# Kernel optimization log

Measured on AMD Instinct MI355X. Metric: run time of the kernel, lower is better.

## Reference

```python
import jax, jax.numpy as jnp
import numpy as np

B, N, F_IN, H, MH, STEPS = 8192, 9, 15, 128, 256, 4
E_PER = 16
MASK_IDX = jnp.arange(8)  # mask = [True]*8 + [False]


def setup_inputs() -> dict:
    key = jax.random.key(0)
    ks = jax.random.split(key, 24)
    s = 0.05
    inp = {
        "obs": jax.random.normal(ks[0], (B, 135), jnp.float32),
        "edges": jax.random.randint(ks[1], (B, 2, E_PER), 0, N, jnp.int32),
        "enc_W": jax.random.normal(ks[2], (F_IN, H), jnp.float32) * s,
        "enc_b": jax.random.normal(ks[3], (H,), jnp.float32) * s,
        "msg_W1": jax.random.normal(ks[4], (STEPS, 2 * H, MH), jnp.float32) * s,
        "msg_b1": jax.random.normal(ks[5], (STEPS, MH), jnp.float32) * s,
        "msg_W2": jax.random.normal(ks[6], (STEPS, MH, MH), jnp.float32) * s,
        "msg_b2": jax.random.normal(ks[7], (STEPS, MH), jnp.float32) * s,
        "msg_W3": jax.random.normal(ks[8], (STEPS, MH, H), jnp.float32) * s,
        "msg_b3": jax.random.normal(ks[9], (STEPS, H), jnp.float32) * s,
        "gru_Wi": jax.random.normal(ks[10], (STEPS, H, 3 * H), jnp.float32) * s,
        "gru_Wh": jax.random.normal(ks[11], (STEPS, H, 3 * H), jnp.float32) * s,
        "gru_bi": jax.random.normal(ks[12], (STEPS, 3 * H), jnp.float32) * s,
        "gru_bh": jax.random.normal(ks[13], (STEPS, 3 * H), jnp.float32) * s,
        "dec_W1": jax.random.normal(ks[14], (H, MH), jnp.float32) * s,
        "dec_b1": jax.random.normal(ks[15], (MH,), jnp.float32) * s,
        "dec_W2": jax.random.normal(ks[16], (MH, MH), jnp.float32) * s,
        "dec_b2": jax.random.normal(ks[17], (MH,), jnp.float32) * s,
        "dec_W3": jax.random.normal(ks[18], (MH, 1), jnp.float32) * s,
        "dec_b3": jax.random.normal(ks[19], (1,), jnp.float32) * s,
    }
    return inp


def reference(obs, edges, enc_W, enc_b, msg_W1, msg_b1, msg_W2, msg_b2,
              msg_W3, msg_b3, gru_Wi, gru_Wh, gru_bi, gru_bh,
              dec_W1, dec_b1, dec_W2, dec_b2, dec_W3, dec_b3):
    BN = B * N
    x = obs.reshape(BN, F_IN)                       # [B*N, 15]
    x = jnp.tanh(x @ enc_W + enc_b)                 # encoder -> [B*N, H]

    # flatten per-graph edges into a global edge list, then add self-loops
    offsets = (jnp.arange(B, dtype=jnp.int32) * N)[:, None, None]
    eg = edges + offsets                            # [B, 2, 16]
    loops = jnp.arange(BN, dtype=jnp.int32)
    src = jnp.concatenate([eg[:, 0, :].reshape(-1), loops])  # x_j (source)
    dst = jnp.concatenate([eg[:, 1, :].reshape(-1), loops])  # x_i (target)
    deg = jax.ops.segment_sum(jnp.ones_like(dst, dtype=x.dtype), dst,
                              num_segments=BN)      # >=1 due to self-loops

    for s in range(STEPS):
        m = jnp.concatenate([x[dst], x[src]], axis=-1)       # [E, 2H]
        m = jnp.tanh(m @ msg_W1[s] + msg_b1[s])
        m = jnp.tanh(m @ msg_W2[s] + msg_b2[s])
        m = m @ msg_W3[s] + msg_b3[s]                        # [E, H]
        aggr = jax.ops.segment_sum(m, dst, num_segments=BN) / deg[:, None]
        # GRUCell(input=aggr, hidden=x), PyTorch gate order (r, z, n)
        gi = aggr @ gru_Wi[s] + gru_bi[s]
        gh = x @ gru_Wh[s] + gru_bh[s]
        ir, iz, inn = jnp.split(gi, 3, axis=-1)
        hr, hz, hn = jnp.split(gh, 3, axis=-1)
        r = jax.nn.sigmoid(ir + hr)
        z = jax.nn.sigmoid(iz + hz)
        n = jnp.tanh(inn + r * hn)
        x = (1.0 - z) * n + z * x

    d = jnp.tanh(x @ dec_W1 + dec_b1)
    d = jnp.tanh(d @ dec_W2 + dec_b2)
    d = d @ dec_W3 + dec_b3                                  # [B*N, 1]
    out = d.reshape(B, N)
    return out[:, MASK_IDX]                                  # [B, 8]
```

## Files before the change

### kernel.cpp

```cpp
#include <hip/hip_runtime.h>
#include <hip/hip_bf16.h>
#include <math.h>

#define BGR   8192
#define NND   9
#define BN    73728
#define NE    131072
#define ETOT  204800
#define H     128
#define MH    256
#define FIN   15

typedef __bf16 bf16_t;
typedef bf16_t bf16x8 __attribute__((ext_vector_type(8)));
typedef float  f32x4  __attribute__((ext_vector_type(4)));

__device__ __forceinline__ unsigned short f2bf(float f) {
    unsigned int u = __float_as_uint(f);
    u += 0x7fff + ((u >> 16) & 1);
    return (unsigned short)(u >> 16);
}
__device__ __forceinline__ bf16x8 as_frag(int4 v) {
    union { int4 i; bf16x8 f; } u; u.i = v; return u.f;
}
__device__ __forceinline__ float fast_tanh(float v) {
    float e = __expf(2.0f * v);
    return 1.0f - __fdividef(2.0f, e + 1.0f);
}
__device__ __forceinline__ int sw_off(int m, int k) {
    return m * 256 + ((((k >> 3) ^ (m & 7)) << 3) | (k & 7));
}

__global__ void deg_kernel(const int* __restrict__ edges, float* __restrict__ inv_deg) {
    int g = blockIdx.x * 256 + threadIdx.x;
    if (g >= BGR) return;
    int cnt[NND];
#pragma unroll
    for (int n = 0; n < NND; ++n) cnt[n] = 1;
    for (int j = 0; j < 16; ++j) {
        int d = edges[g * 32 + 16 + j];
#pragma unroll
        for (int n = 0; n < NND; ++n) cnt[n] += (d == n) ? 1 : 0;
    }
#pragma unroll
    for (int n = 0; n < NND; ++n) inv_deg[g * NND + n] = 1.0f / (float)cnt[n];
}

__global__ void enc_kernel(const float* __restrict__ obs, const float* __restrict__ W,
                           const float* __restrict__ b, float* __restrict__ x) {
    int tid = blockIdx.x * 256 + threadIdx.x;
    int i = tid >> 7, h = tid & 127;
    float acc = b[h];
#pragma unroll
    for (int k = 0; k < FIN; ++k) acc += obs[i * FIN + k] * W[k * H + h];
    x[i * H + h] = tanhf(acc);
}

__global__ void wt_kernel(const float* __restrict__ W1, const float* __restrict__ W2,
                          const float* __restrict__ W3, const float* __restrict__ Wi,
                          const float* __restrict__ Wh, unsigned short* __restrict__ out) {
    int idx = blockIdx.x * 256 + threadIdx.x;
    float v;
    if (idx < 262144) {
        int s = idx >> 16, r = idx & 65535, n = r >> 8, k = r & 255;
        v = W1[(s << 16) + (k << 8) + n];
    } else if (idx < 524288) {
        int i2 = idx - 262144;
        int s = i2 >> 16, r = i2 & 65535, n = r >> 8, k = r & 255;
        v = W2[(s << 16) + (k << 8) + n];
    } else if (idx < 655360) {
        int i3 = idx - 524288;
        int s = i3 >> 15, r = i3 & 32767, n = r >> 8, k = r & 255;
        v = W3[(s << 15) + (k << 7) + n];
    } else {
        int i4 = idx - 655360;
        int s = i4 >> 17, rr = i4 & 131071;
        int p = rr >> 8, k = rr & 255;
        int w = p >> 7, rem = p & 127;
        int gate = rem >> 5, hh = (rem >> 4) & 1, c = rem & 15;
        int h = w * 32 + hh * 16 + c;
        const int sb = s * 49152;
        if (gate == 0)      v = (k < 128) ? Wi[sb + k * 384 + h]       : Wh[sb + (k - 128) * 384 + h];
        else if (gate == 1) v = (k < 128) ? Wi[sb + k * 384 + 128 + h] : Wh[sb + (k - 128) * 384 + 128 + h];
        else if (gate == 2) v = (k < 128) ? Wi[sb + k * 384 + 256 + h] : 0.f;
        else                v = (k < 128) ? 0.f                        : Wh[sb + (k - 128) * 384 + 256 + h];
    }
    out[idx] = f2bf(v);
}

__global__ __launch_bounds__(256, 2) void msg_mfma(
        const float* __restrict__ x, const int* __restrict__ edges,
        const unsigned short* __restrict__ W1T, const float* __restrict__ b1,
        const unsigned short* __restrict__ W2T, const float* __restrict__ b2,
        const unsigned short* __restrict__ W3T, const float* __restrict__ b3,
        float* __restrict__ aggr) {
    __shared__ unsigned short bufA[64 * 256];
    __shared__ unsigned short bufB[64 * 256];
    const int t  = threadIdx.x;
    const int e0 = blockIdx.x * 64;
    const int wv = t >> 6;
    const int ln = t & 63;
    const int lrow = ln & 15;
    const int lq   = ln >> 4;

    {
        const int row  = t >> 1;
        const int e    = row & 63;
        const int side = row >> 6;
        const int eg   = e0 + e;
        int node;
        if (eg < NE) {
            int g = eg >> 4, j = eg & 15;
            node = g * NND + (side ? edges[g * 32 + j] : edges[g * 32 + 16 + j]);
        } else {
            node = eg - NE;
        }
        const int kpart = (t & 1) * 64;
        const float* xs = x + (size_t)node * H + kpart;
        const int kbase = side * 128 + kpart;
#pragma unroll
        for (int i = 0; i < 16; ++i) {
            float4 v = *(const float4*)(xs + i * 4);
            int k0 = kbase + i * 4;
            ushort4 o;
            o.x = f2bf(v.x); o.y = f2bf(v.y); o.z = f2bf(v.z); o.w = f2bf(v.w);
            *(ushort4*)(bufA + sw_off(e, k0)) = o;
        }
    }
    __syncthreads();

    const f32x4 zero = {0.f, 0.f, 0.f, 0.f};
    const int nbase = wv * 64;

    {
        f32x4 acc[4][4];
#pragma unroll
        for (int i = 0; i < 4; ++i)
#pragma unroll
            for (int j = 0; j < 4; ++j) acc[i][j] = zero;
        for (int kq = 0; kq < 8; ++kq) {
            const int ko = kq * 32 + lq * 8;
            bf16x8 af[4], bfr[4];
#pragma unroll
            for (int tm = 0; tm < 4; ++tm)
                af[tm] = as_frag(*(const int4*)(bufA + sw_off(tm * 16 + lrow, ko)));
#pragma unroll
            for (int tn = 0; tn < 4; ++tn)
                bfr[tn] = as_frag(*(const int4*)(W1T + (size_t)(nbase + tn * 16 + lrow) * 256 + ko));
#pragma unroll
            for (int tm = 0; tm < 4; ++tm)
#pragma unroll
                for (int tn = 0; tn < 4; ++tn)
                    acc[tm][tn] = __builtin_amdgcn_mfma_f32_16x16x32_bf16(af[tm], bfr[tn], acc[tm][tn], 0, 0, 0);
        }
#pragma unroll
        for (int tn = 0; tn < 4; ++tn) {
            const int n = nbase + tn * 16 + lrow;
            const float bias = b1[n];
#pragma unroll
            for (int tm = 0; tm < 4; ++tm)
#pragma unroll
                for (int r = 0; r < 4; ++r) {
                    const int m = tm * 16 + lq * 4 + r;
                    bufB[sw_off(m, n)] = f2bf(fast_tanh(acc[tm][tn][r] + bias));
                }
        }
    }
    __syncthreads();

    {
        f32x4 acc[4][4];
#pragma unroll
        for (int i = 0; i < 4; ++i)
#pragma unroll
            for (int j = 0; j < 4; ++j) acc[i][j] = zero;
        for (int kq = 0; kq < 8; ++kq) {
            const int ko = kq * 32 + lq * 8;
            bf16x8 af[4], bfr[4];
#pragma unroll
            for (int tm = 0; tm < 4; ++tm)
                af[tm] = as_frag(*(const int4*)(bufB + sw_off(tm * 16 + lrow, ko)));
#pragma unroll
            for (int tn = 0; tn < 4; ++tn)
                bfr[tn] = as_frag(*(const int4*)(W2T + (size_t)(nbase + tn * 16 + lrow) * 256 + ko));
#pragma unroll
            for (int tm = 0; tm < 4; ++tm)
#pragma unroll
                for (int tn = 0; tn < 4; ++tn)
                    acc[tm][tn] = __builtin_amdgcn_mfma_f32_16x16x32_bf16(af[tm], bfr[tn], acc[tm][tn], 0, 0, 0);
        }
#pragma unroll
        for (int tn = 0; tn < 4; ++tn) {
            const int n = nbase + tn * 16 + lrow;
            const float bias = b2[n];
#pragma unroll
            for (int tm = 0; tm < 4; ++tm)
#pragma unroll
                for (int r = 0; r < 4; ++r) {
                    const int m = tm * 16 + lq * 4 + r;
                    bufA[sw_off(m, n)] = f2bf(fast_tanh(acc[tm][tn][r] + bias));
                }
        }
    }
    __syncthreads();

    {
        const int mh = wv >> 1;
        const int nh = wv & 1;
        f32x4 acc[2][4];
#pragma unroll
        for (int i = 0; i < 2; ++i)
#pragma unroll
            for (int j = 0; j < 4; ++j) acc[i][j] = zero;
        for (int kq = 0; kq < 8; ++kq) {
            const int ko = kq * 32 + lq * 8;
            bf16x8 af[2], bfr[4];
#pragma unroll
            for (int tm = 0; tm < 2; ++tm)
                af[tm] = as_frag(*(const int4*)(bufA + sw_off(mh * 32 + tm * 16 + lrow, ko)));
#pragma unroll
            for (int tn = 0; tn < 4; ++tn)
                bfr[tn] = as_frag(*(const int4*)(W3T + (size_t)(nh * 64 + tn * 16 + lrow) * 256 + ko));
#pragma unroll
            for (int tm = 0; tm < 2; ++tm)
#pragma unroll
                for (int tn = 0; tn < 4; ++tn)
                    acc[tm][tn] = __builtin_amdgcn_mfma_f32_16x16x32_bf16(af[tm], bfr[tn], acc[tm][tn], 0, 0, 0);
        }
#pragma unroll
        for (int tm = 0; tm < 2; ++tm)
#pragma unroll
            for (int r = 0; r < 4; ++r) {
                const int m = mh * 32 + tm * 16 + lq * 4 + r;
                const int eg = e0 + m;
                int d;
                if (eg < NE) {
                    int g = eg >> 4;
                    d = g * NND + edges[g * 32 + 16 + (eg & 15)];
                } else {
                    d = eg - NE;
                }
                float* ap = aggr + (size_t)d * H;
#pragma unroll
                for (int tn = 0; tn < 4; ++tn) {
                    const int n = nh * 64 + tn * 16 + lrow;
                    atomicAdd(ap + n, acc[tm][tn][r] + b3[n]);
                }
            }
    }
}

__global__ __launch_bounds__(256, 2) void gru_mfma(
        float* __restrict__ x, float* __restrict__ aggr, const float* __restrict__ inv_deg,
        const unsigned short* __restrict__ WG,
        const float* __restrict__ bi, const float* __restrict__ bh) {
    __shared__ unsigned short bufA[64 * 256];
    const int t = threadIdx.x;
    const int n0 = blockIdx.x * 64;
    const int wv = t >> 6, ln = t & 63, lrow = ln & 15, lq = ln >> 4;

    {
        const int m = t >> 2;
        const int q = t & 3;
        const int node = n0 + m;
        const int k0 = q * 64;
        const float scale = (q < 2) ? inv_deg[node] : 1.f;
        const float* src = (q < 2) ? (aggr + (size_t)node * H + k0)
                                   : (x    + (size_t)node * H + (k0 - 128));
#pragma unroll
        for (int i = 0; i < 16; ++i) {
            float4 v = *(const float4*)(src + i * 4);
            ushort4 o;
            o.x = f2bf(v.x * scale); o.y = f2bf(v.y * scale);
            o.z = f2bf(v.z * scale); o.w = f2bf(v.w * scale);
            *(ushort4*)(bufA + sw_off(m, k0 + i * 4)) = o;
        }
    }
    __syncthreads();

    const f32x4 zero = {0.f, 0.f, 0.f, 0.f};
    f32x4 acc[4][8];
#pragma unroll
    for (int i = 0; i < 4; ++i)
#pragma unroll
        for (int j = 0; j < 8; ++j) acc[i][j] = zero;

    for (int kq = 0; kq < 8; ++kq) {
        const int ko = kq * 32 + lq * 8;
        bf16x8 af[4], bfr[8];
#pragma unroll
        for (int tm = 0; tm < 4; ++tm)
            af[tm] = as_frag(*(const int4*)(bufA + sw_off(tm * 16 + lrow, ko)));
#pragma unroll
        for (int jt = 0; jt < 8; ++jt)
            bfr[jt] = as_frag(*(const int4*)(WG + (size_t)(wv * 128 + jt * 16 + lrow) * 256 + ko));
#pragma unroll
        for (int tm = 0; tm < 4; ++tm)
#pragma unroll
            for (int jt = 0; jt < 8; ++jt)
                acc[tm][jt] = __builtin_amdgcn_mfma_f32_16x16x32_bf16(af[tm], bfr[jt], acc[tm][jt], 0, 0, 0);
    }

#pragma unroll
    for (int hh = 0; hh < 2; ++hh) {
        const int h = wv * 32 + hh * 16 + lrow;
        const float b_r = bi[h] + bh[h];
        const float b_z = bi[128 + h] + bh[128 + h];
        const float b_n = bi[256 + h];
        const float b_h = bh[256 + h];
#pragma unroll
        for (int tm = 0; tm < 4; ++tm) {
#pragma unroll
            for (int r = 0; r < 4; ++r) {
                const int node = n0 + tm * 16 + lq * 4 + r;
                const float irhr = acc[tm][0 + hh][r] + b_r;
                const float izhz = acc[tm][2 + hh][r] + b_z;
                const float inn  = acc[tm][4 + hh][r] + b_n;
                const float hn   = acc[tm][6 + hh][r] + b_h;
                const float rg = 1.f / (1.f + expf(-irhr));
                const float zg = 1.f / (1.f + expf(-izhz));
                const float ng = tanhf(inn + rg * hn);
                const float xo = x[(size_t)node * H + h];
                x[(size_t)node * H + h] = (1.f - zg) * ng + zg * xo;
                aggr[(size_t)node * H + h] = 0.f;
            }
        }
    }
}

__global__ __launch_bounds__(256, 2) void dec_kernel(
        const float* __restrict__ x,
        const float* __restrict__ W1, const float* __restrict__ b1,
        const float* __restrict__ W2, const float* __restrict__ b2,
        const float* __restrict__ W3, const float* __restrict__ b3,
        float* __restrict__ out) {
    __shared__ float bufA[256 * 36];
    __shared__ float d1[256 * 36];
    const int t = threadIdx.x;
    const int id0 = blockIdx.x * 32;

    {
        const int n = t & 31;
        const int k0 = (t >> 5) * 16;
        const int id = id0 + n;
        const int node = (id >> 3) * NND + (id & 7);
#pragma unroll
        for (int i = 0; i < 16; ++i)
            bufA[(k0 + i) * 36 + n] = x[node * H + k0 + i];
    }
    __syncthreads();

    const int cg = t & 63, ng = t >> 6;
    const int c0 = cg * 4, nb = ng * 8;
    float acc[32];

#pragma unroll
    for (int i = 0; i < 32; ++i) acc[i] = 0.f;
    for (int k = 0; k < 128; ++k) {
        const float4 w  = *(const float4*)(W1 + k * 256 + c0);
        const float4 a0 = *(const float4*)(bufA + k * 36 + nb);
        const float4 a1 = *(const float4*)(bufA + k * 36 + nb + 4);
        const float wv[4] = {w.x, w.y, w.z, w.w};
        const float av[8] = {a0.x, a0.y, a0.z, a0.w, a1.x, a1.y, a1.z, a1.w};
#pragma unroll
        for (int cc = 0; cc < 4; ++cc)
#pragma unroll
            for (int j = 0; j < 8; ++j) acc[cc * 8 + j] += wv[cc] * av[j];
    }
    __syncthreads();
#pragma unroll
    for (int cc = 0; cc < 4; ++cc) {
        float bv = b1[c0 + cc];
#pragma unroll
        for (int j = 0; j < 8; ++j)
            d1[(c0 + cc) * 36 + nb + j] = tanhf(acc[cc * 8 + j] + bv);
    }
    __syncthreads();

#pragma unroll
    for (int i = 0; i < 32; ++i) acc[i] = 0.f;
    for (int k = 0; k < 256; ++k) {
        const float4 w  = *(const float4*)(W2 + k * 256 + c0);
        const float4 a0 = *(const float4*)(d1 + k * 36 + nb);
        const float4 a1 = *(const float4*)(d1 + k * 36 + nb + 4);
        const float wv[4] = {w.x, w.y, w.z, w.w};
        const float av[8] = {a0.x, a0.y, a0.z, a0.w, a1.x, a1.y, a1.z, a1.w};
#pragma unroll
        for (int cc = 0; cc < 4; ++cc)
#pragma unroll
            for (int j = 0; j < 8; ++j) acc[cc * 8 + j] += wv[cc] * av[j];
    }
#pragma unroll
    for (int cc = 0; cc < 4; ++cc) {
        float bv = b2[c0 + cc];
#pragma unroll
        for (int j = 0; j < 8; ++j)
            bufA[(c0 + cc) * 36 + nb + j] = tanhf(acc[cc * 8 + j] + bv);
    }
    __syncthreads();

    {
        const int n3 = t >> 3, p = t & 7;
        float s = 0.f;
#pragma unroll
        for (int i = 0; i < 32; ++i) {
            int k = p * 32 + i;
            s += bufA[k * 36 + n3] * W3[k];
        }
        s += __shfl_down(s, 4, 8);
        s += __shfl_down(s, 2, 8);
        s += __shfl_down(s, 1, 8);
        if (p == 0) out[id0 + n3] = s + b3[0];
    }
}

extern "C" void kernel_launch(void* const* d_in, const int* in_sizes, int n_in,
                              void* d_out, int out_size, void* d_ws, size_t ws_size,
                              hipStream_t stream) {
    const float* obs    = (const float*)d_in[0];
    const int*   edges  = (const int*)  d_in[1];
    const float* enc_W  = (const float*)d_in[2];
    const float* enc_b  = (const float*)d_in[3];
    const float* msg_W1 = (const float*)d_in[4];
    const float* msg_b1 = (const float*)d_in[5];
    const float* msg_W2 = (const float*)d_in[6];
    const float* msg_b2 = (const float*)d_in[7];
    const float* msg_W3 = (const float*)d_in[8];
    const float* msg_b3 = (const float*)d_in[9];
    const float* gru_Wi = (const float*)d_in[10];
    const float* gru_Wh = (const float*)d_in[11];
    const float* gru_bi = (const float*)d_in[12];
    const float* gru_bh = (const float*)d_in[13];
    const float* dec_W1 = (const float*)d_in[14];
    const float* dec_b1 = (const float*)d_in[15];
    const float* dec_W2 = (const float*)d_in[16];
    const float* dec_b2 = (const float*)d_in[17];
    const float* dec_W3 = (const float*)d_in[18];
    const float* dec_b3 = (const float*)d_in[19];

    float* x       = (float*)d_ws;
    float* aggr    = x + (size_t)BN * H;
    float* inv_deg = aggr + (size_t)BN * H;
    unsigned short* wbf = (unsigned short*)(inv_deg + BN);

    hipMemsetAsync(aggr, 0, (size_t)BN * H * sizeof(float), stream);
    deg_kernel<<<(BGR + 255) / 256, 256, 0, stream>>>(edges, inv_deg);
    wt_kernel<<<1179648 / 256, 256, 0, stream>>>(msg_W1, msg_W2, msg_W3, gru_Wi, gru_Wh, wbf);
    enc_kernel<<<BN * H / 256, 256, 0, stream>>>(obs, enc_W, enc_b, x);

    for (int s = 0; s < 4; ++s) {
        const unsigned short* W1T = wbf + (size_t)s * 65536;
        const unsigned short* W2T = wbf + 262144 + (size_t)s * 65536;
        const unsigned short* W3T = wbf + 524288 + (size_t)s * 32768;
        const unsigned short* WGs = wbf + 655360 + (size_t)s * 131072;
        msg_mfma<<<ETOT / 64, 256, 0, stream>>>(
            x, edges,
            W1T, msg_b1 + (size_t)s * 256,
            W2T, msg_b2 + (size_t)s * 256,
            W3T, msg_b3 + (size_t)s * 128,
            aggr);
        gru_mfma<<<BN / 64, 256, 0, stream>>>(
            x, aggr, inv_deg, WGs,
            gru_bi + (size_t)s * 384, gru_bh + (size_t)s * 384);
    }

    dec_kernel<<<BGR * 8 / 32, 256, 0, stream>>>(
        x, dec_W1, dec_b1, dec_W2, dec_b2, dec_W3, dec_b3, (float*)d_out);
}
```

Before: 1.646 ms.

## Port decoder to bf16 MFMA, halve msg LDS, move bias b3 into GRU

The fp32 scalar decoder becomes a bf16 MFMA kernel, with its weights pre-transposed to bf16 in wt_kernel. msg_mfma drops from two LDS buffers to one, using extra barriers so it can run 4 blocks per CU instead of 2. The msg_b3 bias is no longer added inside every per-edge atomicAdd; it is applied once per node in gru_mfma's load phase as aggr*inv_deg + b3, which is algebraically equivalent because the average over degree includes the bias once. Packed bf16 conversion intrinsics replace the per-element rounding, and the decoder now runs at bf16 precision, which adds numerical error.

```diff
diff --git a/kernel.cpp b/kernel.cpp
--- a/kernel.cpp
+++ b/kernel.cpp
@@ -20,6 +20,11 @@
     u += 0x7fff + ((u >> 16) & 1);
     return (unsigned short)(u >> 16);
 }
+__device__ __forceinline__ unsigned int pkbf(float a, float b) {
+    union { __hip_bfloat162 h; unsigned int u; } un;
+    un.h = __float22bfloat162_rn(make_float2(a, b));
+    return un.u;
+}
 __device__ __forceinline__ bf16x8 as_frag(int4 v) {
     union { int4 i; bf16x8 f; } u; u.i = v; return u.f;
 }
@@ -58,7 +63,8 @@
 
 __global__ void wt_kernel(const float* __restrict__ W1, const float* __restrict__ W2,
                           const float* __restrict__ W3, const float* __restrict__ Wi,
-                          const float* __restrict__ Wh, unsigned short* __restrict__ out) {
+                          const float* __restrict__ Wh, const float* __restrict__ dW1,
+                          const float* __restrict__ dW2, unsigned short* __restrict__ out) {
     int idx = blockIdx.x * 256 + threadIdx.x;
     float v;
     if (idx < 262144) {
@@ -72,7 +78,7 @@
         int i3 = idx - 524288;
         int s = i3 >> 15, r = i3 & 32767, n = r >> 8, k = r & 255;
         v = W3[(s << 15) + (k << 7) + n];
-    } else {
+    } else if (idx < 1179648) {
         int i4 = idx - 655360;
         int s = i4 >> 17, rr = i4 & 131071;
         int p = rr >> 8, k = rr & 255;
@@ -84,18 +90,25 @@
         else if (gate == 1) v = (k < 128) ? Wi[sb + k * 384 + 128 + h] : Wh[sb + (k - 128) * 384 + 128 + h];
         else if (gate == 2) v = (k < 128) ? Wi[sb + k * 384 + 256 + h] : 0.f;
         else                v = (k < 128) ? 0.f                        : Wh[sb + (k - 128) * 384 + 256 + h];
+    } else if (idx < 1212416) {
+        int i5 = idx - 1179648;
+        int n = i5 >> 7, k = i5 & 127;
+        v = dW1[k * 256 + n];
+    } else {
+        int i6 = idx - 1212416;
+        int n = i6 >> 8, k = i6 & 255;
+        v = dW2[k * 256 + n];
     }
     out[idx] = f2bf(v);
 }
 
-__global__ __launch_bounds__(256, 2) void msg_mfma(
+__global__ __launch_bounds__(256, 4) void msg_mfma(
         const float* __restrict__ x, const int* __restrict__ edges,
         const unsigned short* __restrict__ W1T, const float* __restrict__ b1,
         const unsigned short* __restrict__ W2T, const float* __restrict__ b2,
-        const unsigned short* __restrict__ W3T, const float* __restrict__ b3,
+        const unsigned short* __restrict__ W3T,
         float* __restrict__ aggr) {
-    __shared__ unsigned short bufA[64 * 256];
-    __shared__ unsigned short bufB[64 * 256];
+    __shared__ unsigned short buf[64 * 256];
     const int t  = threadIdx.x;
     const int e0 = blockIdx.x * 64;
     const int wv = t >> 6;
@@ -121,10 +134,9 @@
 #pragma unroll
         for (int i = 0; i < 16; ++i) {
             float4 v = *(const float4*)(xs + i * 4);
-            int k0 = kbase + i * 4;
-            ushort4 o;
-            o.x = f2bf(v.x); o.y = f2bf(v.y); o.z = f2bf(v.z); o.w = f2bf(v.w);
-            *(ushort4*)(bufA + sw_off(e, k0)) = o;
+            uint2 o;
+            o.x = pkbf(v.x, v.y); o.y = pkbf(v.z, v.w);
+            *(uint2*)(buf + sw_off(e, kbase + i * 4)) = o;
         }
     }
     __syncthreads();
@@ -143,7 +155,7 @@
             bf16x8 af[4], bfr[4];
 #pragma unroll
             for (int tm = 0; tm < 4; ++tm)
-                af[tm] = as_frag(*(const int4*)(bufA + sw_off(tm * 16 + lrow, ko)));
+                af[tm] = as_frag(*(const int4*)(buf + sw_off(tm * 16 + lrow, ko)));
 #pragma unroll
             for (int tn = 0; tn < 4; ++tn)
                 bfr[tn] = as_frag(*(const int4*)(W1T + (size_t)(nbase + tn * 16 + lrow) * 256 + ko));
@@ -153,6 +165,7 @@
                 for (int tn = 0; tn < 4; ++tn)
                     acc[tm][tn] = __builtin_amdgcn_mfma_f32_16x16x32_bf16(af[tm], bfr[tn], acc[tm][tn], 0, 0, 0);
         }
+        __syncthreads();
 #pragma unroll
         for (int tn = 0; tn < 4; ++tn) {
             const int n = nbase + tn * 16 + lrow;
@@ -162,7 +175,7 @@
 #pragma unroll
                 for (int r = 0; r < 4; ++r) {
                     const int m = tm * 16 + lq * 4 + r;
-                    bufB[sw_off(m, n)] = f2bf(fast_tanh(acc[tm][tn][r] + bias));
+                    buf[sw_off(m, n)] = f2bf(fast_tanh(acc[tm][tn][r] + bias));
                 }
         }
     }
@@ -179,7 +192,7 @@
             bf16x8 af[4], bfr[4];
 #pragma unroll
             for (int tm = 0; tm < 4; ++tm)
-                af[tm] = as_frag(*(const int4*)(bufB + sw_off(tm * 16 + lrow, ko)));
+                af[tm] = as_frag(*(const int4*)(buf + sw_off(tm * 16 + lrow, ko)));
 #pragma unroll
             for (int tn = 0; tn < 4; ++tn)
                 bfr[tn] = as_frag(*(const int4*)(W2T + (size_t)(nbase + tn * 16 + lrow) * 256 + ko));
@@ -189,6 +202,7 @@
                 for (int tn = 0; tn < 4; ++tn)
                     acc[tm][tn] = __builtin_amdgcn_mfma_f32_16x16x32_bf16(af[tm], bfr[tn], acc[tm][tn], 0, 0, 0);
         }
+        __syncthreads();
 #pragma unroll
         for (int tn = 0; tn < 4; ++tn) {
             const int n = nbase + tn * 16 + lrow;
@@ -198,7 +212,7 @@
 #pragma unroll
                 for (int r = 0; r < 4; ++r) {
                     const int m = tm * 16 + lq * 4 + r;
-                    bufA[sw_off(m, n)] = f2bf(fast_tanh(acc[tm][tn][r] + bias));
+                    buf[sw_off(m, n)] = f2bf(fast_tanh(acc[tm][tn][r] + bias));
                 }
         }
     }
@@ -217,7 +231,7 @@
             bf16x8 af[2], bfr[4];
 #pragma unroll
             for (int tm = 0; tm < 2; ++tm)
-                af[tm] = as_frag(*(const int4*)(bufA + sw_off(mh * 32 + tm * 16 + lrow, ko)));
+                af[tm] = as_frag(*(const int4*)(buf + sw_off(mh * 32 + tm * 16 + lrow, ko)));
 #pragma unroll
             for (int tn = 0; tn < 4; ++tn)
                 bfr[tn] = as_frag(*(const int4*)(W3T + (size_t)(nh * 64 + tn * 16 + lrow) * 256 + ko));
@@ -244,7 +258,7 @@
 #pragma unroll
                 for (int tn = 0; tn < 4; ++tn) {
                     const int n = nh * 64 + tn * 16 + lrow;
-                    atomicAdd(ap + n, acc[tm][tn][r] + b3[n]);
+                    atomicAdd(ap + n, acc[tm][tn][r]);
                 }
             }
     }
@@ -252,7 +266,7 @@
 
 __global__ __launch_bounds__(256, 2) void gru_mfma(
         float* __restrict__ x, float* __restrict__ aggr, const float* __restrict__ inv_deg,
-        const unsigned short* __restrict__ WG,
+        const unsigned short* __restrict__ WG, const float* __restrict__ b3m,
         const float* __restrict__ bi, const float* __restrict__ bh) {
     __shared__ unsigned short bufA[64 * 256];
     const int t = threadIdx.x;
@@ -264,16 +278,26 @@
         const int q = t & 3;
         const int node = n0 + m;
         const int k0 = q * 64;
-        const float scale = (q < 2) ? inv_deg[node] : 1.f;
-        const float* src = (q < 2) ? (aggr + (size_t)node * H + k0)
-                                   : (x    + (size_t)node * H + (k0 - 128));
-#pragma unroll
-        for (int i = 0; i < 16; ++i) {
-            float4 v = *(const float4*)(src + i * 4);
-            ushort4 o;
-            o.x = f2bf(v.x * scale); o.y = f2bf(v.y * scale);
-            o.z = f2bf(v.z * scale); o.w = f2bf(v.w * scale);
-            *(ushort4*)(bufA + sw_off(m, k0 + i * 4)) = o;
+        if (q < 2) {
+            const float scale = inv_deg[node];
+            const float* src = aggr + (size_t)node * H + k0;
+#pragma unroll
+            for (int i = 0; i < 16; ++i) {
+                float4 v = *(const float4*)(src + i * 4);
+                const float4 bb = *(const float4*)(b3m + k0 + i * 4);
+                v.x = v.x * scale + bb.x; v.y = v.y * scale + bb.y;
+                v.z = v.z * scale + bb.z; v.w = v.w * scale + bb.w;
+                uint2 o; o.x = pkbf(v.x, v.y); o.y = pkbf(v.z, v.w);
+                *(uint2*)(bufA + sw_off(m, k0 + i * 4)) = o;
+            }
+        } else {
+            const float* src = x + (size_t)node * H + (k0 - 128);
+#pragma unroll
+            for (int i = 0; i < 16; ++i) {
+                float4 v = *(const float4*)(src + i * 4);
+                uint2 o; o.x = pkbf(v.x, v.y); o.y = pkbf(v.z, v.w);
+                *(uint2*)(bufA + sw_off(m, k0 + i * 4)) = o;
+            }
         }
     }
     __syncthreads();
@@ -328,89 +352,120 @@
     }
 }
 
-__global__ __launch_bounds__(256, 2) void dec_kernel(
+__global__ __launch_bounds__(256, 4) void dec_mfma(
         const float* __restrict__ x,
-        const float* __restrict__ W1, const float* __restrict__ b1,
-        const float* __restrict__ W2, const float* __restrict__ b2,
+        const unsigned short* __restrict__ W1T, const float* __restrict__ b1,
+        const unsigned short* __restrict__ W2T, const float* __restrict__ b2,
         const float* __restrict__ W3, const float* __restrict__ b3,
         float* __restrict__ out) {
-    __shared__ float bufA[256 * 36];
-    __shared__ float d1[256 * 36];
+    __shared__ unsigned short buf[64 * 256];
     const int t = threadIdx.x;
-    const int id0 = blockIdx.x * 32;
-
-    {
-        const int n = t & 31;
-        const int k0 = (t >> 5) * 16;
-        const int id = id0 + n;
+    const int id0 = blockIdx.x * 64;
+    const int wv = t >> 6, ln = t & 63, lrow = ln & 15, lq = ln >> 4;
+    const int nbase = wv * 64;
+
+    {
+        const int m = t >> 2, q = t & 3;
+        const int id = id0 + m;
         const int node = (id >> 3) * NND + (id & 7);
-#pragma unroll
-        for (int i = 0; i < 16; ++i)
-            bufA[(k0 + i) * 36 + n] = x[node * H + k0 + i];
-    }
-    __syncthreads();
-
-    const int cg = t & 63, ng = t >> 6;
-    const int c0 = cg * 4, nb = ng * 8;
-    float acc[32];
-
-#pragma unroll
-    for (int i = 0; i < 32; ++i) acc[i] = 0.f;
-    for (int k = 0; k < 128; ++k) {
-        const float4 w  = *(const float4*)(W1 + k * 256 + c0);
-        const float4 a0 = *(const float4*)(bufA + k * 36 + nb);
-        const float4 a1 = *(const float4*)(bufA + k * 36 + nb + 4);
-        const float wv[4] = {w.x, w.y, w.z, w.w};
-        const float av[8] = {a0.x, a0.y, a0.z, a0.w, a1.x, a1.y, a1.z, a1.w};
-#pragma unroll
-        for (int cc = 0; cc < 4; ++cc)
-#pragma unroll
-            for (int j = 0; j < 8; ++j) acc[cc * 8 + j] += wv[cc] * av[j];
-    }
-    __syncthreads();
-#pragma unroll
-    for (int cc = 0; cc < 4; ++cc) {
-        float bv = b1[c0 + cc];
-#pragma unroll
-        for (int j = 0; j < 8; ++j)
-            d1[(c0 + cc) * 36 + nb + j] = tanhf(acc[cc * 8 + j] + bv);
-    }
-    __syncthreads();
-
-#pragma unroll
-    for (int i = 0; i < 32; ++i) acc[i] = 0.f;
-    for (int k = 0; k < 256; ++k) {
-        const float4 w  = *(const float4*)(W2 + k * 256 + c0);
-        const float4 a0 = *(const float4*)(d1 + k * 36 + nb);
-        const float4 a1 = *(const float4*)(d1 + k * 36 + nb + 4);
-        const float wv[4] = {w.x, w.y, w.z, w.w};
-        const float av[8] = {a0.x, a0.y, a0.z, a0.w, a1.x, a1.y, a1.z, a1.w};
-#pragma unroll
-        for (int cc = 0; cc < 4; ++cc)
-#pragma unroll
-            for (int j = 0; j < 8; ++j) acc[cc * 8 + j] += wv[cc] * av[j];
-    }
-#pragma unroll
-    for (int cc = 0; cc < 4; ++cc) {
-        float bv = b2[c0 + cc];
-#pragma unroll
-        for (int j = 0; j < 8; ++j)
-            bufA[(c0 + cc) * 36 + nb + j] = tanhf(acc[cc * 8 + j] + bv);
-    }
-    __syncthreads();
-
-    {
-        const int n3 = t >> 3, p = t & 7;
+        const float* src = x + (size_t)node * H + q * 32;
+#pragma unroll
+        for (int i = 0; i < 8; ++i) {
+            float4 v = *(const float4*)(src + i * 4);
+            uint2 o; o.x = pkbf(v.x, v.y); o.y = pkbf(v.z, v.w);
+            *(uint2*)(buf + sw_off(m, q * 32 + i * 4)) = o;
+        }
+    }
+    __syncthreads();
+
+    const f32x4 zero = {0.f, 0.f, 0.f, 0.f};
+
+    {
+        f32x4 acc[4][4];
+#pragma unroll
+        for (int i = 0; i < 4; ++i)
+#pragma unroll
+            for (int j = 0; j < 4; ++j) acc[i][j] = zero;
+        for (int kq = 0; kq < 4; ++kq) {
+            const int ko = kq * 32 + lq * 8;
+            bf16x8 af[4], bfr[4];
+#pragma unroll
+            for (int tm = 0; tm < 4; ++tm)
+                af[tm] = as_frag(*(const int4*)(buf + sw_off(tm * 16 + lrow, ko)));
+#pragma unroll
+            for (int tn = 0; tn < 4; ++tn)
+                bfr[tn] = as_frag(*(const int4*)(W1T + (size_t)(nbase + tn * 16 + lrow) * 128 + ko));
+#pragma unroll
+            for (int tm = 0; tm < 4; ++tm)
+#pragma unroll
+                for (int tn = 0; tn < 4; ++tn)
+                    acc[tm][tn] = __builtin_amdgcn_mfma_f32_16x16x32_bf16(af[tm], bfr[tn], acc[tm][tn], 0, 0, 0);
+        }
+        __syncthreads();
+#pragma unroll
+        for (int tn = 0; tn < 4; ++tn) {
+            const int n = nbase + tn * 16 + lrow;
+            const float bias = b1[n];
+#pragma unroll
+            for (int tm = 0; tm < 4; ++tm)
+#pragma unroll
+                for (int r = 0; r < 4; ++r) {
+                    const int m = tm * 16 + lq * 4 + r;
+                    buf[sw_off(m, n)] = f2bf(fast_tanh(acc[tm][tn][r] + bias));
+                }
+        }
+    }
+    __syncthreads();
+
+    {
+        f32x4 acc[4][4];
+#pragma unroll
+        for (int i = 0; i < 4; ++i)
+#pragma unroll
+            for (int j = 0; j < 4; ++j) acc[i][j] = zero;
+        for (int kq = 0; kq < 8; ++kq) {
+            const int ko = kq * 32 + lq * 8;
+            bf16x8 af[4], bfr[4];
+#pragma unroll
+            for (int tm = 0; tm < 4; ++tm)
+                af[tm] = as_frag(*(const int4*)(buf + sw_off(tm * 16 + lrow, ko)));
+#pragma unroll
+            for (int tn = 0; tn < 4; ++tn)
+                bfr[tn] = as_frag(*(const int4*)(W2T + (size_t)(nbase + tn * 16 + lrow) * 256 + ko));
+#pragma unroll
+            for (int tm = 0; tm < 4; ++tm)
+#pragma unroll
+                for (int tn = 0; tn < 4; ++tn)
+                    acc[tm][tn] = __builtin_amdgcn_mfma_f32_16x16x32_bf16(af[tm], bfr[tn], acc[tm][tn], 0, 0, 0);
+        }
+        __syncthreads();
+#pragma unroll
+        for (int tn = 0; tn < 4; ++tn) {
+            const int n = nbase + tn * 16 + lrow;
+            const float bias = b2[n];
+#pragma unroll
+            for (int tm = 0; tm < 4; ++tm)
+#pragma unroll
+                for (int r = 0; r < 4; ++r) {
+                    const int m = tm * 16 + lq * 4 + r;
+                    buf[sw_off(m, n)] = f2bf(fast_tanh(acc[tm][tn][r] + bias));
+                }
+        }
+    }
+    __syncthreads();
+
+    {
+        const int m = t >> 2, p = t & 3;
         float s = 0.f;
 #pragma unroll
-        for (int i = 0; i < 32; ++i) {
-            int k = p * 32 + i;
-            s += bufA[k * 36 + n3] * W3[k];
-        }
-        s += __shfl_down(s, 4, 8);
-        s += __shfl_down(s, 2, 8);
-        s += __shfl_down(s, 1, 8);
-        if (p == 0) out[id0 + n3] = s + b3[0];
+        for (int i = 0; i < 64; ++i) {
+            const int k = p * 64 + i;
+            const float a = __uint_as_float((unsigned int)buf[sw_off(m, k)] << 16);
+            s += a * W3[k];
+        }
+        s += __shfl_xor(s, 1);
+        s += __shfl_xor(s, 2);
+        if (p == 0) out[id0 + m] = s + b3[0];
     }
 }
 
@@ -445,7 +500,8 @@
 
     hipMemsetAsync(aggr, 0, (size_t)BN * H * sizeof(float), stream);
     deg_kernel<<<(BGR + 255) / 256, 256, 0, stream>>>(edges, inv_deg);
-    wt_kernel<<<1179648 / 256, 256, 0, stream>>>(msg_W1, msg_W2, msg_W3, gru_Wi, gru_Wh, wbf);
+    wt_kernel<<<1277952 / 256, 256, 0, stream>>>(msg_W1, msg_W2, msg_W3, gru_Wi, gru_Wh,
+                                                 dec_W1, dec_W2, wbf);
     enc_kernel<<<BN * H / 256, 256, 0, stream>>>(obs, enc_W, enc_b, x);
 
     for (int s = 0; s < 4; ++s) {
@@ -457,13 +513,13 @@
             x, edges,
             W1T, msg_b1 + (size_t)s * 256,
             W2T, msg_b2 + (size_t)s * 256,
-            W3T, msg_b3 + (size_t)s * 128,
+            W3T,
             aggr);
         gru_mfma<<<BN / 64, 256, 0, stream>>>(
-            x, aggr, inv_deg, WGs,
+            x, aggr, inv_deg, WGs, msg_b3 + (size_t)s * 128,
             gru_bi + (size_t)s * 384, gru_bh + (size_t)s * 384);
     }
 
-    dec_kernel<<<BGR * 8 / 32, 256, 0, stream>>>(
-        x, dec_W1, dec_b1, dec_W2, dec_b2, dec_W3, dec_b3, (float*)d_out);
-}
+    dec_mfma<<<BGR * 8 / 64, 256, 0, stream>>>(
+        x, wbf + 1179648, dec_b1, wbf + 1212416, dec_b2, dec_W3, dec_b3, (float*)d_out);
+}
```

Result: slower. 1.740 ms (+5.7%).
